# Performance work log

Measured on AMD Instinct MI355X. Metric: run time of the kernel, lower is better.

The kernel has to match this reference:

```python
import jax, jax.numpy as jnp
import numpy as np

B, S, D = 1, 2048, 2048
H, KVH = 32, 8
HD = D // H          # 64
N_REP = H // KVH     # 4
ROPE_THETA = 10000.0
NEG = -1e9


def setup_inputs() -> dict:
    key = jax.random.key(0)
    ks = jax.random.split(key, 8)
    x = jax.random.normal(ks[0], (B, S, D), dtype=jnp.float32)
    # RoPE tables: freqs_cis[t, j] = exp(i * t * theta^{-2j/HD}), j in [0, HD/2)
    inv_freq = 1.0 / (ROPE_THETA ** (jnp.arange(0, HD, 2, dtype=jnp.float32) / HD))
    angles = jnp.arange(S, dtype=jnp.float32)[:, None] * inv_freq[None, :]  # (S, HD/2)
    freqs_cos = jnp.cos(angles)
    freqs_sin = jnp.sin(angles)
    # causal additive mask (S, S)
    mask = jnp.where(jnp.tril(jnp.ones((S, S), dtype=bool)), 0.0, NEG).astype(jnp.float32)
    sc = 0.02
    wq = jax.random.normal(ks[1], (D, H * HD), dtype=jnp.float32) * sc
    wk = jax.random.normal(ks[2], (D, KVH * HD), dtype=jnp.float32) * sc
    wv = jax.random.normal(ks[3], (D, KVH * HD), dtype=jnp.float32) * sc
    wo = jax.random.normal(ks[4], (H * HD, D), dtype=jnp.float32) * sc
    fw = jax.random.normal(ks[5], (HD, HD), dtype=jnp.float32) * sc
    fb = jnp.zeros((HD,), dtype=jnp.float32)
    return {"x": x, "freqs_cos": freqs_cos, "freqs_sin": freqs_sin, "mask": mask,
            "wq": wq, "wk": wk, "wv": wv, "wo": wo, "fw": fw, "fb": fb,
            "start_pos": 0}


def _rope(t, cos, sin):
    # t: (B, S, h, HD) -> complex rotate pairs along last dim
    tr = t.reshape(*t.shape[:-1], HD // 2, 2)
    c = cos[None, :, None, :]  # (1, S, 1, HD/2)
    s = sin[None, :, None, :]
    re = tr[..., 0] * c - tr[..., 1] * s
    im = tr[..., 0] * s + tr[..., 1] * c
    return jnp.stack([re, im], axis=-1).reshape(t.shape)


def reference(x, freqs_cos, freqs_sin, mask, wq, wk, wv, wo, fw, fb, start_pos):
    b, s, _ = x.shape
    xq = (x @ wq).reshape(b, s, H, HD)
    xk = (x @ wk).reshape(b, s, KVH, HD)
    xv = (x @ wv).reshape(b, s, KVH, HD)
    xq = _rope(xq, freqs_cos, freqs_sin)
    xk = _rope(xk, freqs_cos, freqs_sin)
    # GQA: repeat kv heads (repeat_interleave on head dim)
    keys = jnp.repeat(xk, N_REP, axis=2)    # (b, s, H, HD)
    values = jnp.repeat(xv, N_REP, axis=2)
    q = xq.transpose(0, 2, 1, 3)            # (b, H, s, HD)
    k = keys.transpose(0, 2, 1, 3)
    v = values.transpose(0, 2, 1, 3)
    scores = jnp.einsum("bhqd,bhkd->bhqk", q, k) / np.sqrt(HD).astype(np.float32)
    scores = scores + mask[None, None, :, :]
    probs = jax.nn.softmax(scores.astype(jnp.float32), axis=-1).astype(q.dtype)
    out = jnp.einsum("bhqk,bhkd->bhqd", probs, v)  # (b, H, s, HD)
    # shared per-head FFN: Linear(HD, HD) + SiLU, vectorized over heads
    out = jax.nn.silu(out @ fw + fb)
    out = out.transpose(0, 2, 1, 3).reshape(b, s, H * HD)
    return out @ wo
```

## Files before the change

### kernel.cpp

```cpp
#include <hip/hip_runtime.h>
#include <stdint.h>

#define S_LEN 2048
#define DMODEL 2048
#define NH 32
#define NKV 8
#define HD 64

typedef __attribute__((ext_vector_type(8))) __bf16 bf16x8;
typedef __attribute__((ext_vector_type(4))) float f32x4;
typedef __attribute__((ext_vector_type(16))) float f32x16;

__device__ __forceinline__ unsigned short f2bf(float f) {
    union { float f; uint32_t u; } v; v.f = f;
    uint32_t u = v.u;
    u += 0x7FFFu + ((u >> 16) & 1u);
    return (unsigned short)(u >> 16);
}

__device__ __forceinline__ uint32_t cvt_pk_bf16(float lo, float hi) {
    uint32_t r;
    asm("v_cvt_pk_bf16_f32 %0, %1, %2" : "=v"(r) : "v"(lo), "v"(hi));
    return r;
}

#define GLDS16(g, l)                                                          \
    __builtin_amdgcn_global_load_lds(                                         \
        (const __attribute__((address_space(1))) unsigned int*)(g),           \
        (__attribute__((address_space(3))) unsigned int*)(l), 16, 0, 0)

__device__ const int kUQT[24] = {15,15,7,14,14,13,13,6,12,12,11,11,5,10,10,9,9,4,8,8,3,2,1,0};
__device__ const int kUCH[24] = {0,1,0,0,1,0,1,0,0,1,0,1,0,0,1,0,1,0,0,1,0,0,0,0};
__device__ const int kUSP[24] = {1,1,0,1,1,1,1,0,1,1,1,1,0,1,1,1,1,0,1,1,0,0,0,0};

__global__ void prep_kernel(
    const float* __restrict__ wq, const float* __restrict__ wk,
    const float* __restrict__ wv, const float* __restrict__ wo,
    const float* __restrict__ fw, const float* __restrict__ x,
    unsigned short* __restrict__ wqkvT, unsigned short* __restrict__ woT,
    unsigned short* __restrict__ fwT, unsigned short* __restrict__ xb) {
    const int z = blockIdx.z;
    const int tx = threadIdx.x, ty = threadIdx.y;
    if (z == 5) {
        int base = (blockIdx.y * 64 + blockIdx.x) * 1024 + (ty * 32 + tx) * 4;
        float4 a = *(const float4*)&x[base];
        ushort4 o;
        o.x = f2bf(a.x); o.y = f2bf(a.y); o.z = f2bf(a.z); o.w = f2bf(a.w);
        *(ushort4*)&xb[base] = o;
        return;
    }
    __shared__ float tile[32][33];
    const float* src;
    unsigned short* dst;
    int R, C;
    if (z == 0)      { src = wq; dst = wqkvT;                       R = 2048; C = 2048; }
    else if (z == 1) { src = wk; dst = wqkvT + (size_t)2048 * 2048; R = 2048; C = 512;  if (blockIdx.x >= 16) return; }
    else if (z == 2) { src = wv; dst = wqkvT + (size_t)2560 * 2048; R = 2048; C = 512;  if (blockIdx.x >= 16) return; }
    else if (z == 3) { src = wo; dst = woT;                         R = 2048; C = 2048; }
    else             { src = fw; dst = fwT;                         R = 64;   C = 64;   if (blockIdx.x >= 2 || blockIdx.y >= 2) return; }
    int c0 = blockIdx.x * 32, r0 = blockIdx.y * 32;
#pragma unroll
    for (int i = 0; i < 32; i += 8)
        tile[ty + i][tx] = src[(size_t)(r0 + ty + i) * C + c0 + tx];
    __syncthreads();
#pragma unroll
    for (int i = 0; i < 32; i += 8)
        dst[(size_t)(c0 + ty + i) * R + r0 + tx] = f2bf(tile[tx][ty + i]);
}

template <int MODE>
__global__ __launch_bounds__(256) void gemm_bt_kernel(
    const unsigned short* __restrict__ A, const unsigned short* __restrict__ BT,
    float* __restrict__ C0, unsigned short* __restrict__ Qb,
    unsigned short* __restrict__ Kb, unsigned short* __restrict__ VT,
    const float* __restrict__ fcos, const float* __restrict__ fsin,
    int M, int N, int K) {
    __shared__ unsigned short As[3][128 * 32];
    __shared__ unsigned short Bs[3][64 * 32];
    const int t = threadIdx.x;
    const int lane = t & 63, wave = t >> 6;
    const int wr = wave >> 1, wc = wave & 1;
    const int gx = gridDim.x;
    const int nwg = gx * gridDim.y;
    const int wg = blockIdx.y * gx + blockIdx.x;
    const int swz = (wg & 7) * (nwg >> 3) + (wg >> 3);
    const int m0 = (swz % gx) * 128, n0 = (swz / gx) * 64;
    const int l15 = lane & 15, lhi = lane >> 4;
    f32x4 acc[4][2] = {};
    const unsigned short* ga = A + (size_t)(m0 + (t >> 2)) * K + (t & 3) * 8;
    const unsigned short* gb = BT + (size_t)(n0 + (t >> 2)) * K + (t & 3) * 8;
    const int nk = K >> 5;

#define GSTAGE(buf, kt)                                                       \
    {                                                                         \
        const int k0_ = (kt) * 32;                                            \
        GLDS16(ga + k0_, &As[buf][t * 8]);                                    \
        GLDS16(ga + (size_t)64 * K + k0_, &As[buf][t * 8 + 64 * 32]);         \
        if (t < 256) GLDS16(gb + k0_, &Bs[buf][t * 8]);                       \
    }

    GSTAGE(0, 0);
    GSTAGE(1, 1);

    int cb = 0, pfb = 2;
#pragma unroll 1
    for (int kt = 0; kt < nk; ++kt) {
        if (kt + 1 < nk) asm volatile("s_waitcnt vmcnt(3)" ::: "memory");
        else             asm volatile("s_waitcnt vmcnt(0)" ::: "memory");
        __builtin_amdgcn_s_barrier();
        __builtin_amdgcn_sched_barrier(0);
        if (kt + 2 < nk) GSTAGE(pfb, kt + 2);
        pfb = (pfb == 2) ? 0 : pfb + 1;
        const int mycb = cb;
        cb = (cb == 2) ? 0 : cb + 1;
        bf16x8 af[4], bfr[2];
#pragma unroll
        for (int m = 0; m < 4; m++)
            af[m] = *(const bf16x8*)&As[mycb][(wr * 64 + m * 16 + l15) * 32 + lhi * 8];
#pragma unroll
        for (int n = 0; n < 2; n++)
            bfr[n] = *(const bf16x8*)&Bs[mycb][(wc * 32 + n * 16 + l15) * 32 + lhi * 8];
#pragma unroll
        for (int m = 0; m < 4; m++)
#pragma unroll
            for (int n = 0; n < 2; n++)
                acc[m][n] = __builtin_amdgcn_mfma_f32_16x16x32_bf16(
                    af[m], bfr[n], acc[m][n], 0, 0, 0);
    }
#undef GSTAGE
    if (MODE == 0) {
#pragma unroll
        for (int m = 0; m < 4; m++) {
            int row = m0 + wr * 64 + m * 16 + lhi * 4;
#pragma unroll
            for (int n = 0; n < 2; n++) {
                int col = n0 + wc * 32 + n * 16 + l15;
#pragma unroll
                for (int r = 0; r < 4; r++)
                    C0[(size_t)(row + r) * N + col] = acc[m][n][r];
            }
        }
    } else {
        const int nblk = n0 >> 6;
        if (nblk < 40) {
            const float CS = 0.125f * 1.44269504f;
            const bool isQ = (nblk < 32);
            unsigned short* dst = isQ ? Qb + (size_t)nblk * (S_LEN * HD)
                                      : Kb + (size_t)(nblk - 32) * (S_LEN * HD);
#pragma unroll
            for (int m = 0; m < 4; m++) {
#pragma unroll
                for (int n = 0; n < 2; n++) {
                    int col = wc * 32 + n * 16 + l15;
                    int i = col >> 1;
                    float sgn = (col & 1) ? 1.f : -1.f;
#pragma unroll
                    for (int r = 0; r < 4; r++) {
                        int s = m0 + wr * 64 + m * 16 + lhi * 4 + r;
                        float c = fcos[s * 32 + i], sn = fsin[s * 32 + i];
                        float v = acc[m][n][r];
                        float pv = __shfl_xor(v, 1);
                        float o = fmaf(pv, sgn * sn, v * c);
                        if (isQ) o *= CS;
                        dst[(size_t)s * HD + col] = f2bf(o);
                    }
                }
            }
        } else {
            const int kvh = nblk - 40;
            unsigned short* ldsT = (unsigned short*)As;
            __syncthreads();
#pragma unroll
            for (int m = 0; m < 4; m++)
#pragma unroll
                for (int n = 0; n < 2; n++) {
                    int d = wc * 32 + n * 16 + l15;
#pragma unroll
                    for (int r = 0; r < 4; r++) {
                        int sl = wr * 64 + m * 16 + lhi * 4 + r;
                        ldsT[d * 130 + sl] = f2bf(acc[m][n][r]);
                    }
                }
            __syncthreads();
            const int d = t >> 2, sc = (t & 3) * 32;
            unsigned short* dst = VT + ((size_t)kvh * HD + d) * S_LEN + m0 + sc;
            const unsigned short* srcl = &ldsT[d * 130 + sc];
#pragma unroll
            for (int j = 0; j < 16; j++)
                ((uint32_t*)dst)[j] = *(const uint32_t*)&srcl[2 * j];
        }
    }
}

__global__ __launch_bounds__(256) void flash_kernel(
    const unsigned short* __restrict__ Q, const unsigned short* __restrict__ Kg,
    const unsigned short* __restrict__ VTg, unsigned short* __restrict__ O,
    float* __restrict__ Opart, float* __restrict__ ML) {
    __shared__ unsigned short Ks[3][2048];
    __shared__ unsigned short Vs[3][2048];
    const int t = threadIdx.x, lane = t & 63, wave = t >> 6;
    const int l31 = lane & 31, hi = lane >> 5;
    const int bid = blockIdx.x;
    const int h = bid & 31, u = bid >> 5;
    const int qt = kUQT[u], ch = kUCH[u], sp = kUSP[u];
    const int kvh = h >> 2;

    const int kt0 = sp ? ch * (2 * qt + 2) : 0;
    const int ktN = kt0 + (sp ? (2 * qt + 2) : (4 * qt + 4));

    const int srow = t >> 3;
    const int scol = ((t & 7) * 8) ^ ((srow & 7) * 8);
    const unsigned short* gk = Kg + ((size_t)kvh * S_LEN + srow) * HD + scol;
    const int vrow = t >> 2;
    const int vcol = (((t & 3) ^ (vrow & 3)) * 8);
    const unsigned short* gv = VTg + ((size_t)kvh * HD + vrow) * S_LEN + vcol;

    const int q0 = qt * 128;
    const int qw0 = q0 + wave * 32;
    const int q = qw0 + l31;

    const unsigned short* qp = Q + ((size_t)h * S_LEN + q) * HD + hi * 8;
    bf16x8 qf0 = *(const bf16x8*)(qp);
    bf16x8 qf1 = *(const bf16x8*)(qp + 16);
    bf16x8 qf2 = *(const bf16x8*)(qp + 32);
    bf16x8 qf3 = *(const bf16x8*)(qp + 48);

    f32x16 oacc0 = {}, oacc1 = {};
    float mrun = -1e30f, lrun = 0.f;

#define FSTAGE(buf, kt)                                                       \
    {                                                                         \
        const size_t kv_ = (size_t)(kt) * 32;                                 \
        GLDS16(gk + kv_ * HD, &Ks[buf][t * 8]);                               \
        GLDS16(gv + kv_, &Vs[buf][t * 8]);                                    \
    }

    FSTAGE(0, kt0);
    FSTAGE(1, kt0 + 1);

    int cb = 0, pfb = 2;
#pragma unroll 1
    for (int kt = kt0; kt < ktN; ++kt) {
        if (kt + 1 < ktN) asm volatile("s_waitcnt vmcnt(2)" ::: "memory");
        else              asm volatile("s_waitcnt vmcnt(0)" ::: "memory");
        __builtin_amdgcn_s_barrier();
        __builtin_amdgcn_sched_barrier(0);
        if (kt + 2 < ktN) FSTAGE(pfb, kt + 2);
        pfb = (pfb == 2) ? 0 : pfb + 1;
        const int kv0 = kt * 32;
        const int mycb = cb;
        cb = (cb == 2) ? 0 : cb + 1;
        if (kv0 > qw0 + 31) continue;
        const unsigned short* ksb = Ks[mycb];
        const unsigned short* vsb = Vs[mycb];
        const int sw = (l31 & 7) * 8;
        f32x16 s0 = {};
#pragma unroll
        for (int kc = 0; kc < 4; kc++) {
            bf16x8 k0 = *(const bf16x8*)&ksb[l31 * 64 + ((16 * kc + 8 * hi) ^ sw)];
            bf16x8 qc = (kc == 0) ? qf0 : (kc == 1) ? qf1 : (kc == 2) ? qf2 : qf3;
            s0 = __builtin_amdgcn_mfma_f32_32x32x16_bf16(k0, qc, s0, 0, 0, 0);
        }
        float p0[16];
        if (kv0 + 31 <= qw0) {
#pragma unroll
            for (int r = 0; r < 16; r++) p0[r] = s0[r];
        } else {
#pragma unroll
            for (int r = 0; r < 16; r++) {
                int rr = (r & 3) + 8 * (r >> 2) + 4 * hi;
                p0[r] = (kv0 + rr <= q) ? s0[r] : -1e30f;
            }
        }
        float t8[8];
#pragma unroll
        for (int r = 0; r < 8; r++) t8[r] = fmaxf(p0[r], p0[r + 8]);
        float lm = fmaxf(fmaxf(fmaxf(t8[0], t8[4]), fmaxf(t8[1], t8[5])),
                         fmaxf(fmaxf(t8[2], t8[6]), fmaxf(t8[3], t8[7])));
        if (!__all(lm - mrun <= 8.f)) {
            float rm = fmaxf(lm, __shfl_xor(lm, 32));
            float mnew = fmaxf(mrun, rm);
            float sc = exp2f(mrun - mnew);
            mrun = mnew;
            lrun *= sc;
            oacc0 *= sc;
            oacc1 *= sc;
        }
#pragma unroll
        for (int r = 0; r < 16; r++) p0[r] = exp2f(p0[r] - mrun);
        float sA = 0.f, sB = 0.f;
#pragma unroll
        for (int r = 0; r < 4; r++) {
            sA += p0[r] + p0[r + 4];
            sB += p0[r + 8] + p0[r + 12];
        }
        lrun += sA + sB;
        bf16x8 pf[2];
#pragma unroll
        for (int kc = 0; kc < 2; kc++) {
            const int sub = kc * 8;
            uint32_t Wl0 = cvt_pk_bf16(p0[sub + 0], p0[sub + 1]);
            uint32_t Wl1 = cvt_pk_bf16(p0[sub + 2], p0[sub + 3]);
            uint32_t Wh0 = cvt_pk_bf16(p0[sub + 4], p0[sub + 5]);
            uint32_t Wh1 = cvt_pk_bf16(p0[sub + 6], p0[sub + 7]);
            uint32_t sw0 = hi ? Wl0 : Wh0, sw1 = hi ? Wl1 : Wh1;
            uint32_t rc0 = __shfl_xor((int)sw0, 32);
            uint32_t rc1 = __shfl_xor((int)sw1, 32);
            uint32_t kp0 = hi ? Wh0 : Wl0, kp1 = hi ? Wh1 : Wl1;
            uint32_t F0 = hi ? rc0 : kp0;
            uint32_t F1 = hi ? rc1 : kp1;
            uint32_t F2 = hi ? kp0 : rc0;
            uint32_t F3 = hi ? kp1 : rc1;
            uint4 fu = {F0, F1, F2, F3};
            pf[kc] = *(const bf16x8*)&fu;
        }
#pragma unroll
        for (int kc = 0; kc < 2; kc++) {
            const int vs0 = ((kc * 2 + hi) ^ (l31 & 3)) * 8;
            bf16x8 v0 = *(const bf16x8*)&vsb[l31 * 32 + vs0];
            bf16x8 v1 = *(const bf16x8*)&vsb[(32 + l31) * 32 + vs0];
            oacc0 = __builtin_amdgcn_mfma_f32_32x32x16_bf16(v0, pf[kc], oacc0, 0, 0, 0);
            oacc1 = __builtin_amdgcn_mfma_f32_32x32x16_bf16(v1, pf[kc], oacc1, 0, 0, 0);
        }
    }
#undef FSTAGE
    lrun += __shfl_xor(lrun, 32);
    const int qrow = wave * 32 + l31;
    if (sp) {
        const int pidx = (h * 8 + (qt - 8)) * 2 + ch;
        float* po = Opart + ((size_t)pidx * 128 + qrow) * 64 + 4 * hi;
#pragma unroll
        for (int g = 0; g < 4; g++) {
            float4 a = {oacc0[4 * g], oacc0[4 * g + 1], oacc0[4 * g + 2], oacc0[4 * g + 3]};
            *(float4*)(po + 8 * g) = a;
            float4 b = {oacc1[4 * g], oacc1[4 * g + 1], oacc1[4 * g + 2], oacc1[4 * g + 3]};
            *(float4*)(po + 32 + 8 * g) = b;
        }
        if (hi == 0) {
            ML[((size_t)pidx * 128 + qrow) * 2] = mrun;
            ML[((size_t)pidx * 128 + qrow) * 2 + 1] = lrun;
        }
    } else {
        float rinv = 1.f / lrun;
        unsigned short* ob = O + ((size_t)h * S_LEN + q) * HD + 4 * hi;
#pragma unroll
        for (int g = 0; g < 4; g++) {
            uint32_t a0 = cvt_pk_bf16(oacc0[4 * g] * rinv, oacc0[4 * g + 1] * rinv);
            uint32_t a1 = cvt_pk_bf16(oacc0[4 * g + 2] * rinv, oacc0[4 * g + 3] * rinv);
            uint2 u0 = {a0, a1};
            *(uint2*)(ob + 8 * g) = u0;
            uint32_t b0 = cvt_pk_bf16(oacc1[4 * g] * rinv, oacc1[4 * g + 1] * rinv);
            uint32_t b1 = cvt_pk_bf16(oacc1[4 * g + 2] * rinv, oacc1[4 * g + 3] * rinv);
            uint2 u1 = {b0, b1};
            *(uint2*)(ob + 32 + 8 * g) = u1;
        }
    }
}

__global__ __launch_bounds__(256) void fw_silu_kernel(
    const unsigned short* __restrict__ AT, const unsigned short* __restrict__ fwT,
    const float* __restrict__ fb, const float* __restrict__ Opart,
    const float* __restrict__ ML, unsigned short* __restrict__ h2) {
    const int t = threadIdx.x, lane = t & 63, wave = t >> 6;
    const int l15 = lane & 15, lhi = lane >> 4;
    const int r0 = blockIdx.x * 64 + wave * 16;
    const int row = r0 + l15;
    const int hh = row >> 11, s = row & (S_LEN - 1);
    bf16x8 a0, a1;
    if (s < 1024) {
        const unsigned short* ap = AT + (size_t)row * HD + lhi * 8;
        a0 = *(const bf16x8*)ap;
        a1 = *(const bf16x8*)(ap + 32);
    } else {
        const int qt = s >> 7, qrow = s & 127;
        const int pidx = (hh * 8 + (qt - 8)) * 2;
        const float* mlp = ML + ((size_t)pidx * 128 + qrow) * 2;
        const float* mlq = ML + ((size_t)(pidx + 1) * 128 + qrow) * 2;
        float mA = mlp[0], lA = mlp[1], mB = mlq[0], lB = mlq[1];
        float mm = fmaxf(mA, mB);
        float wA = exp2f(mA - mm), wB = exp2f(mB - mm);
        float rv = 1.f / (lA * wA + lB * wB);
        const float* pA = Opart + ((size_t)pidx * 128 + qrow) * 64;
        const float* pB = pA + 8192;
#pragma unroll
        for (int half = 0; half < 2; half++) {
            int db = half * 32 + lhi * 8;
            float4 x0 = *(const float4*)&pA[db], x1 = *(const float4*)&pA[db + 4];
            float4 y0 = *(const float4*)&pB[db], y1 = *(const float4*)&pB[db + 4];
            uint32_t w0 = cvt_pk_bf16((x0.x * wA + y0.x * wB) * rv, (x0.y * wA + y0.y * wB) * rv);
            uint32_t w1 = cvt_pk_bf16((x0.z * wA + y0.z * wB) * rv, (x0.w * wA + y0.w * wB) * rv);
            uint32_t w2 = cvt_pk_bf16((x1.x * wA + y1.x * wB) * rv, (x1.y * wA + y1.y * wB) * rv);
            uint32_t w3 = cvt_pk_bf16((x1.z * wA + y1.z * wB) * rv, (x1.w * wA + y1.w * wB) * rv);
            uint4 u = {w0, w1, w2, w3};
            if (half == 0) a0 = *(const bf16x8*)&u;
            else           a1 = *(const bf16x8*)&u;
        }
    }
    f32x4 acc[4] = {};
#pragma unroll
    for (int nb = 0; nb < 4; nb++) {
        const unsigned short* bp = fwT + (size_t)(nb * 16 + l15) * HD + lhi * 8;
        bf16x8 b0 = *(const bf16x8*)bp;
        bf16x8 b1 = *(const bf16x8*)(bp + 32);
        acc[nb] = __builtin_amdgcn_mfma_f32_16x16x32_bf16(a0, b0, acc[nb], 0, 0, 0);
        acc[nb] = __builtin_amdgcn_mfma_f32_16x16x32_bf16(a1, b1, acc[nb], 0, 0, 0);
    }
#pragma unroll
    for (int nb = 0; nb < 4; nb++) {
        int col = nb * 16 + l15;
        float bias = fb[col];
#pragma unroll
        for (int r = 0; r < 4; r++) {
            int orow = r0 + lhi * 4 + r;
            int os = orow & (S_LEN - 1), oh = orow >> 11;
            float xv = acc[nb][r] + bias;
            float sg = 1.f / (1.f + exp2f(-xv * 1.44269504f));
            h2[(size_t)os * DMODEL + oh * HD + col] = f2bf(xv * sg);
        }
    }
}

extern "C" void kernel_launch(void* const* d_in, const int* in_sizes, int n_in,
                              void* d_out, int out_size, void* d_ws, size_t ws_size,
                              hipStream_t stream) {
    const float* x = (const float*)d_in[0];
    const float* fcos = (const float*)d_in[1];
    const float* fsin = (const float*)d_in[2];
    const float* wq = (const float*)d_in[4];
    const float* wk = (const float*)d_in[5];
    const float* wv = (const float*)d_in[6];
    const float* wo = (const float*)d_in[7];
    const float* fw = (const float*)d_in[8];
    const float* fb = (const float*)d_in[9];
    float* out = (float*)d_out;

    char* ws = (char*)d_ws;
    size_t off = 0;
    auto alloc = [&](size_t bytes) {
        void* p = ws + off;
        off += (bytes + 255) & ~(size_t)255;
        return p;
    };
    unsigned short* wqkvT = (unsigned short*)alloc((size_t)3072 * 2048 * 2);
    unsigned short* woT   = (unsigned short*)alloc((size_t)2048 * 2048 * 2);
    unsigned short* fwT   = (unsigned short*)alloc((size_t)64 * 64 * 2);
    unsigned short* Qb    = (unsigned short*)alloc((size_t)NH * S_LEN * HD * 2);
    unsigned short* Kb    = (unsigned short*)alloc((size_t)NKV * S_LEN * HD * 2);
    unsigned short* VT    = (unsigned short*)alloc((size_t)NKV * HD * S_LEN * 2);
    unsigned short* xb    = (unsigned short*)alloc((size_t)2048 * 2048 * 2);
    float*          ML    = (float*)alloc((size_t)512 * 128 * 2 * 4);
    unsigned short* attn  = (unsigned short*)alloc((size_t)NH * S_LEN * HD * 2);
    float*          Opart = (float*)alloc((size_t)512 * 128 * 64 * 4);
    unsigned short* h2 = xb;

    prep_kernel<<<dim3(64, 64, 6), dim3(32, 8), 0, stream>>>(
        wq, wk, wv, wo, fw, x, wqkvT, woT, fwT, xb);

    gemm_bt_kernel<1><<<dim3(16, 48), 256, 0, stream>>>(
        xb, wqkvT, nullptr, Qb, Kb, VT, fcos, fsin, 2048, 3072, 2048);

    flash_kernel<<<768, 256, 0, stream>>>(Qb, Kb, VT, attn, Opart, ML);

    fw_silu_kernel<<<1024, 256, 0, stream>>>(attn, fwT, fb, Opart, ML, h2);

    gemm_bt_kernel<0><<<dim3(16, 32), 256, 0, stream>>>(
        h2, woT, out, nullptr, nullptr, nullptr, nullptr, nullptr,
        2048, 2048, 2048);
}
```

Measured before the change: 155.9 us.

## Split flash attention KV range into fixed 16-tile chunks with multi-way merge

Replaces the two-way split used only for the upper half of query tiles with fixed-length KV chunks of 16 tiles. Query tiles from 4 upward are split into 2 to 4 chunks, giving 1280 blocks of near-uniform work instead of 768 unbalanced ones. The fw_silu kernel now merges up to four partial results per row using their saved max and sum values. The cost is more fp32 partial-output traffic, larger workspace buffers and a heavier merge step.

```diff
diff --git a/kernel.cpp b/kernel.cpp
--- a/kernel.cpp
+++ b/kernel.cpp
@@ -29,9 +29,15 @@
         (const __attribute__((address_space(1))) unsigned int*)(g),           \
         (__attribute__((address_space(3))) unsigned int*)(l), 16, 0, 0)
 
-__device__ const int kUQT[24] = {15,15,7,14,14,13,13,6,12,12,11,11,5,10,10,9,9,4,8,8,3,2,1,0};
-__device__ const int kUCH[24] = {0,1,0,0,1,0,1,0,0,1,0,1,0,0,1,0,1,0,0,1,0,0,0,0};
-__device__ const int kUSP[24] = {1,1,0,1,1,1,1,0,1,1,1,1,0,1,1,1,1,0,1,1,0,0,0,0};
+__device__ const int8_t kUQT[40] = {3,4,5,6,7,7,8,8,9,9,10,10,11,11,11,12,12,12,13,13,13,14,14,14,15,15,15,15,
+                                    2,6,10,14, 1,5,9,13, 0,4,8,12};
+__device__ const int8_t kUCH[40] = {0,0,0,0,0,1,0,1,0,1,0,1,0,1,2,0,1,2,0,1,2,0,1,2,0,1,2,3,
+                                    0,1,2,3, 0,1,2,3, 0,1,2,3};
+
+__device__ __forceinline__ int slot_base(int qt) {
+    return (qt < 8) ? (qt - 4) * 2 : (qt < 12) ? 8 + (qt - 8) * 3
+                                               : 20 + (qt - 12) * 4;
+}
 
 __global__ void prep_kernel(
     const float* __restrict__ wq, const float* __restrict__ wk,
@@ -202,11 +208,12 @@
     const int l31 = lane & 31, hi = lane >> 5;
     const int bid = blockIdx.x;
     const int h = bid & 31, u = bid >> 5;
-    const int qt = kUQT[u], ch = kUCH[u], sp = kUSP[u];
+    const int qt = kUQT[u], ch = kUCH[u];
+    const int sp = (qt >= 4);
     const int kvh = h >> 2;
 
-    const int kt0 = sp ? ch * (2 * qt + 2) : 0;
-    const int ktN = kt0 + (sp ? (2 * qt + 2) : (4 * qt + 4));
+    const int kt0 = ch * 16;
+    const int ktN = min(kt0 + 16, 4 * qt + 4);
 
     const int srow = t >> 3;
     const int scol = ((t & 7) * 8) ^ ((srow & 7) * 8);
@@ -327,8 +334,8 @@
     lrun += __shfl_xor(lrun, 32);
     const int qrow = wave * 32 + l31;
     if (sp) {
-        const int pidx = (h * 8 + (qt - 8)) * 2 + ch;
-        float* po = Opart + ((size_t)pidx * 128 + qrow) * 64 + 4 * hi;
+        const int slot = h * 36 + slot_base(qt) + ch;
+        float* po = Opart + ((size_t)slot * 128 + qrow) * 64 + 4 * hi;
 #pragma unroll
         for (int g = 0; g < 4; g++) {
             float4 a = {oacc0[4 * g], oacc0[4 * g + 1], oacc0[4 * g + 2], oacc0[4 * g + 3]};
@@ -337,8 +344,8 @@
             *(float4*)(po + 32 + 8 * g) = b;
         }
         if (hi == 0) {
-            ML[((size_t)pidx * 128 + qrow) * 2] = mrun;
-            ML[((size_t)pidx * 128 + qrow) * 2 + 1] = lrun;
+            ML[((size_t)slot * 128 + qrow) * 2] = mrun;
+            ML[((size_t)slot * 128 + qrow) * 2 + 1] = lrun;
         }
     } else {
         float rinv = 1.f / lrun;
@@ -367,30 +374,49 @@
     const int row = r0 + l15;
     const int hh = row >> 11, s = row & (S_LEN - 1);
     bf16x8 a0, a1;
-    if (s < 1024) {
+    if (s < 512) {
         const unsigned short* ap = AT + (size_t)row * HD + lhi * 8;
         a0 = *(const bf16x8*)ap;
         a1 = *(const bf16x8*)(ap + 32);
     } else {
         const int qt = s >> 7, qrow = s & 127;
-        const int pidx = (hh * 8 + (qt - 8)) * 2;
-        const float* mlp = ML + ((size_t)pidx * 128 + qrow) * 2;
-        const float* mlq = ML + ((size_t)(pidx + 1) * 128 + qrow) * 2;
-        float mA = mlp[0], lA = mlp[1], mB = mlq[0], lB = mlq[1];
-        float mm = fmaxf(mA, mB);
-        float wA = exp2f(mA - mm), wB = exp2f(mB - mm);
-        float rv = 1.f / (lA * wA + lB * wB);
-        const float* pA = Opart + ((size_t)pidx * 128 + qrow) * 64;
-        const float* pB = pA + 8192;
+        const int nc = (qt < 8) ? 2 : (qt < 12) ? 3 : 4;
+        const int slot0 = hh * 36 + slot_base(qt);
+        float mc[4], lc[4];
+#pragma unroll
+        for (int c = 0; c < 4; c++) {
+            if (c < nc) {
+                const float* p = ML + ((size_t)(slot0 + c) * 128 + qrow) * 2;
+                mc[c] = p[0]; lc[c] = p[1];
+            } else { mc[c] = -1e30f; lc[c] = 0.f; }
+        }
+        float mm = fmaxf(fmaxf(mc[0], mc[1]), fmaxf(mc[2], mc[3]));
+        float wgt[4]; float den = 0.f;
+#pragma unroll
+        for (int c = 0; c < 4; c++) {
+            wgt[c] = exp2f(mc[c] - mm);
+            den += lc[c] * wgt[c];
+        }
+        float rv = 1.f / den;
 #pragma unroll
         for (int half = 0; half < 2; half++) {
             int db = half * 32 + lhi * 8;
-            float4 x0 = *(const float4*)&pA[db], x1 = *(const float4*)&pA[db + 4];
-            float4 y0 = *(const float4*)&pB[db], y1 = *(const float4*)&pB[db + 4];
-            uint32_t w0 = cvt_pk_bf16((x0.x * wA + y0.x * wB) * rv, (x0.y * wA + y0.y * wB) * rv);
-            uint32_t w1 = cvt_pk_bf16((x0.z * wA + y0.z * wB) * rv, (x0.w * wA + y0.w * wB) * rv);
-            uint32_t w2 = cvt_pk_bf16((x1.x * wA + y1.x * wB) * rv, (x1.y * wA + y1.y * wB) * rv);
-            uint32_t w3 = cvt_pk_bf16((x1.z * wA + y1.z * wB) * rv, (x1.w * wA + y1.w * wB) * rv);
+            float acc8[8] = {};
+#pragma unroll
+            for (int c = 0; c < 4; c++) {
+                if (c < nc) {
+                    const float* pc = Opart + ((size_t)(slot0 + c) * 128 + qrow) * 64 + db;
+                    float4 x0 = *(const float4*)pc, x1 = *(const float4*)(pc + 4);
+                    acc8[0] += x0.x * wgt[c]; acc8[1] += x0.y * wgt[c];
+                    acc8[2] += x0.z * wgt[c]; acc8[3] += x0.w * wgt[c];
+                    acc8[4] += x1.x * wgt[c]; acc8[5] += x1.y * wgt[c];
+                    acc8[6] += x1.z * wgt[c]; acc8[7] += x1.w * wgt[c];
+                }
+            }
+            uint32_t w0 = cvt_pk_bf16(acc8[0] * rv, acc8[1] * rv);
+            uint32_t w1 = cvt_pk_bf16(acc8[2] * rv, acc8[3] * rv);
+            uint32_t w2 = cvt_pk_bf16(acc8[4] * rv, acc8[5] * rv);
+            uint32_t w3 = cvt_pk_bf16(acc8[6] * rv, acc8[7] * rv);
             uint4 u = {w0, w1, w2, w3};
             if (half == 0) a0 = *(const bf16x8*)&u;
             else           a1 = *(const bf16x8*)&u;
@@ -448,9 +474,9 @@
     unsigned short* Kb    = (unsigned short*)alloc((size_t)NKV * S_LEN * HD * 2);
     unsigned short* VT    = (unsigned short*)alloc((size_t)NKV * HD * S_LEN * 2);
     unsigned short* xb    = (unsigned short*)alloc((size_t)2048 * 2048 * 2);
-    float*          ML    = (float*)alloc((size_t)512 * 128 * 2 * 4);
+    float*          ML    = (float*)alloc((size_t)1152 * 128 * 2 * 4);
     unsigned short* attn  = (unsigned short*)alloc((size_t)NH * S_LEN * HD * 2);
-    float*          Opart = (float*)alloc((size_t)512 * 128 * 64 * 4);
+    float*          Opart = (float*)alloc((size_t)1152 * 128 * 64 * 4);
     unsigned short* h2 = xb;
 
     prep_kernel<<<dim3(64, 64, 6), dim3(32, 8), 0, stream>>>(
@@ -459,7 +485,7 @@
     gemm_bt_kernel<1><<<dim3(16, 48), 256, 0, stream>>>(
         xb, wqkvT, nullptr, Qb, Kb, VT, fcos, fsin, 2048, 3072, 2048);
 
-    flash_kernel<<<768, 256, 0, stream>>>(Qb, Kb, VT, attn, Opart, ML);
+    flash_kernel<<<1280, 256, 0, stream>>>(Qb, Kb, VT, attn, Opart, ML);
 
     fw_silu_kernel<<<1024, 256, 0, stream>>>(attn, fwT, fb, Opart, ML, h2);
 
```

New measurement: 163.4 us. 1.05x slower.
